# Kernel tuning notes

Measured on AMD Instinct MI355X. Metric: run time of the kernel, lower is better.

Reference implementation:

```python
import jax, jax.numpy as jnp
import numpy as np
import math

B, N, D, L = 2, 256, 128, 4
TD = D // 2  # time embed dim
GROUPS = 32

def _interleave_sincos(v):
    # torch: stack((v[...,0::2].sin(), v[...,1::2].cos()), -1).flatten(last two)
    s = jnp.sin(v[..., 0::2])
    c = jnp.cos(v[..., 1::2])
    return jnp.stack([s, c], axis=-1).reshape(v.shape[:-1] + (-1,))

def _pos_embed(coords):
    # PositionEmbeddingSine(num_pos_feats=D//2, normalize=True, scale=2*pi)
    npf = D // 2
    dim_t = jnp.power(10000.0, 2.0 * jnp.floor(jnp.arange(npf, dtype=jnp.float32) / 2.0) / npf)
    scale = 2.0 * math.pi
    py = _interleave_sincos((coords[:, :, 0] * scale)[:, :, None] / dim_t)
    px = _interleave_sincos((coords[:, :, 1] * scale)[:, :, None] / dim_t)
    return jnp.concatenate([py, px], axis=-1)  # (B,N,D)

def _edge_pos_embed(adj):
    # ScalarEmbeddingSine(num_pos_feats=D, normalize=False)
    dim_t = jnp.power(10000.0, 2.0 * jnp.floor(jnp.arange(D, dtype=jnp.float32) / 2.0) / D)
    return _interleave_sincos(adj[:, :, :, None] / dim_t)  # (B,N,N,D)

def _timestep_embedding(t, dim):
    half = dim // 2
    freqs = jnp.exp(-math.log(10000.0) * jnp.arange(half, dtype=jnp.float32) / half)
    args = t.astype(jnp.float32)[:, None] * freqs
    return jnp.concatenate([jnp.cos(args), jnp.sin(args)], axis=-1)  # (B,D)

def _ln(x, s, b, eps=1e-5):
    mu = jnp.mean(x, -1, keepdims=True)
    var = jnp.var(x, -1, keepdims=True)
    return (x - mu) * jax.lax.rsqrt(var + eps) * s + b

def _gn(x, s, b, groups=GROUPS, eps=1e-5):
    # GroupNorm32 over (B, C, H, W)
    bb, c, h, w = x.shape
    xg = x.reshape(bb, groups, c // groups, h, w)
    mu = jnp.mean(xg, (2, 3, 4), keepdims=True)
    var = jnp.var(xg, (2, 3, 4), keepdims=True)
    xg = (xg - mu) * jax.lax.rsqrt(var + eps)
    return xg.reshape(bb, c, h, w) * s[None, :, None, None] + b[None, :, None, None]

def _forward(coords, adj_t, t, node_W, node_b, edge_W, edge_b, te1_W, te1_b, te2_W, te2_b,
             A_W, A_b, B_W, B_b, C_W, C_b, U_W, U_b, V_W, V_b,
             lnh_s, lnh_b, lne_s, lne_b, tl_W, tl_b,
             plo_ln_s, plo_ln_b, plo_W, plo_b, gn_s, gn_b, conv_W, conv_b):
    x = _pos_embed(coords) @ node_W + node_b            # (B,N,D)
    e = _edge_pos_embed(adj_t) @ edge_W + edge_b        # (B,N,N,D)
    te = _timestep_embedding(t, D) @ te1_W + te1_b
    te = jax.nn.relu(te) @ te2_W + te2_b                # (B,TD)
    for i in range(L):
        x_in, e_in = x, e
        # GatedGCNLayer (mode=direct, no internal residual)
        Uh = x @ U_W[i] + U_b[i]
        Vh = x @ V_W[i] + V_b[i]
        gate_input = ((x @ A_W[i] + A_b[i])[:, :, None, :]
                      + (x @ B_W[i] + B_b[i])[:, None, :, :]
                      + (e @ C_W[i] + C_b[i]))          # (B,N,N,D)
        gates = jax.nn.sigmoid(gate_input)
        agg = jnp.einsum('bijd,bjd->bid', gates, Vh)     # sum over neighbors j
        h_new = jax.nn.relu(_ln(Uh + agg, lnh_s[i], lnh_b[i]))
        e_new = jax.nn.relu(_ln(gate_input, lne_s[i], lne_b[i]))
        # time injection into edges: ReLU -> Linear(TD->D)
        e_new = e_new + (jax.nn.relu(te) @ tl_W[i] + tl_b[i])[:, None, None, :]
        # external residuals + per-layer out (LN -> SiLU -> Linear)
        x = x_in + h_new
        e = e_in + jax.nn.silu(_ln(e_new, plo_ln_s[i], plo_ln_b[i])) @ plo_W[i] + plo_b[i]
    eo = jnp.transpose(e, (0, 3, 1, 2))                  # (B,D,N,N)
    eo = jax.nn.relu(_gn(eo, gn_s, gn_b))
    out = jnp.einsum('bdij,do->boij', eo, conv_W) + conv_b[None, :, None, None]
    return out                                           # (B,1,N,N)

def setup_inputs() -> dict:
    key = jax.random.key(0)
    ks = iter(jax.random.split(key, 64))
    def w(shape, scale=0.02):
        return jax.random.normal(next(ks), shape, dtype=jnp.float32) * scale
    f32 = jnp.float32
    return {
        'coords': jax.random.uniform(next(ks), (B, N, 2), dtype=f32),
        'adj_t': jax.random.normal(next(ks), (B, N, N), dtype=f32),
        't': jax.random.uniform(next(ks), (B,), dtype=f32) * 1000.0,
        'node_W': w((D, D)), 'node_b': jnp.zeros((D,), f32),
        'edge_W': w((D, D)), 'edge_b': jnp.zeros((D,), f32),
        'te1_W': w((D, TD)), 'te1_b': jnp.zeros((TD,), f32),
        'te2_W': w((TD, TD)), 'te2_b': jnp.zeros((TD,), f32),
        'A_W': w((L, D, D)), 'A_b': jnp.zeros((L, D), f32),
        'B_W': w((L, D, D)), 'B_b': jnp.zeros((L, D), f32),
        'C_W': w((L, D, D)), 'C_b': jnp.zeros((L, D), f32),
        'U_W': w((L, D, D)), 'U_b': jnp.zeros((L, D), f32),
        'V_W': w((L, D, D)), 'V_b': jnp.zeros((L, D), f32),
        'lnh_s': jnp.ones((L, D), f32), 'lnh_b': jnp.zeros((L, D), f32),
        'lne_s': jnp.ones((L, D), f32), 'lne_b': jnp.zeros((L, D), f32),
        'tl_W': w((L, TD, D)), 'tl_b': jnp.zeros((L, D), f32),
        'plo_ln_s': jnp.ones((L, D), f32), 'plo_ln_b': jnp.zeros((L, D), f32),
        'plo_W': w((L, D, D)), 'plo_b': jnp.zeros((L, D), f32),
        'gn_s': jnp.ones((D,), f32), 'gn_b': jnp.zeros((D,), f32),
        'conv_W': w((D, 1)), 'conv_b': jnp.zeros((1,), f32),
    }

def reference(coords, adj_t, t, node_W, node_b, edge_W, edge_b, te1_W, te1_b, te2_W, te2_b,
              A_W, A_b, B_W, B_b, C_W, C_b, U_W, U_b, V_W, V_b,
              lnh_s, lnh_b, lne_s, lne_b, tl_W, tl_b,
              plo_ln_s, plo_ln_b, plo_W, plo_b, gn_s, gn_b, conv_W, conv_b):
    return _forward(coords, adj_t, t, node_W, node_b, edge_W, edge_b, te1_W, te1_b, te2_W, te2_b,
                    A_W, A_b, B_W, B_b, C_W, C_b, U_W, U_b, V_W, V_b,
                    lnh_s, lnh_b, lne_s, lne_b, tl_W, tl_b,
                    plo_ln_s, plo_ln_b, plo_W, plo_b, gn_s, gn_b, conv_W, conv_b)
```

## Files before the change

kernel.cpp:

```cpp
#include <hip/hip_runtime.h>
#include <hip/hip_bf16.h>

typedef unsigned short u16;
typedef __attribute__((ext_vector_type(8))) short short8;
typedef __attribute__((ext_vector_type(8))) unsigned short ushort8;
typedef __attribute__((ext_vector_type(4))) float f32x4;

#define BB 2
#define NN 256
#define DD 128
#define TDD 64
#define LL 4
#define NGROUP 32
#define NROWS (BB*NN*NN)
#define LDS_STR 68

#define LOG1E4 9.210340371976184f
#define TWO_PI 6.283185307179586f

#define TILE_GEMM(AT, WPTR, ACC) do {                                          \
  _Pragma("unroll 4")                                                          \
  for (int k = 0; k < 128; ++k) {                                              \
    const float4 w4 = *reinterpret_cast<const float4*>((WPTR) + k*128 + tx*4); \
    const float4 a0 = *reinterpret_cast<const float4*>(&(AT)[k*LDS_STR + ty*8]);     \
    const float4 a1 = *reinterpret_cast<const float4*>(&(AT)[k*LDS_STR + ty*8 + 4]); \
    const float av[8] = {a0.x,a0.y,a0.z,a0.w,a1.x,a1.y,a1.z,a1.w};             \
    const float wv[4] = {w4.x,w4.y,w4.z,w4.w};                                 \
    _Pragma("unroll") for (int r = 0; r < 8; ++r)                              \
      _Pragma("unroll") for (int c = 0; c < 4; ++c)                            \
        ACC[r][c] += av[r]*wv[c];                                              \
  }                                                                            \
} while (0)

__device__ __forceinline__ float sigmoidf_(float x) {
  return 1.f / (1.f + __expf(-x));
}

__device__ __forceinline__ u16 f2bf(float f) {
  union { float f; unsigned int u; } c; c.f = f;
  unsigned int r = (c.u + 0x7FFFu + ((c.u >> 16) & 1u)) >> 16;
  return (u16)r;
}

__global__ __launch_bounds__(512) void k_time(
    const float* __restrict__ t,
    const float* __restrict__ te1_W, const float* __restrict__ te1_b,
    const float* __restrict__ te2_W, const float* __restrict__ te2_b,
    const float* __restrict__ tl_W,  const float* __restrict__ tl_b,
    float* __restrict__ tproj) {
  __shared__ float temb[BB][128], h1[BB][64], rt[BB][64];
  const int tid = threadIdx.x;
  const int b  = tid >> 8;
  const int t2 = tid & 255;
  const float tv = t[b];
  if (t2 < 128) {
    int j = t2 & 63;
    float f = expf(-LOG1E4 * (float)j / 64.f);
    float a = tv * f;
    temb[b][t2] = (t2 < 64) ? cosf(a) : sinf(a);
  }
  __syncthreads();
  if (t2 < 64) {
    float acc = te1_b[t2];
#pragma unroll
    for (int k = 0; k < 128; ++k) acc += temb[b][k] * te1_W[k*64 + t2];
    h1[b][t2] = fmaxf(acc, 0.f);
  }
  __syncthreads();
  if (t2 < 64) {
    float acc = te2_b[t2];
#pragma unroll
    for (int k = 0; k < 64; ++k) acc += h1[b][k] * te2_W[k*64 + t2];
    rt[b][t2] = fmaxf(acc, 0.f);
  }
  __syncthreads();
  if (t2 < 128) {
#pragma unroll
    for (int i = 0; i < LL; ++i) {
      float acc = tl_b[i*128 + t2];
#pragma unroll
      for (int k = 0; k < 64; ++k) acc += rt[b][k] * tl_W[(i*64 + k)*128 + t2];
      tproj[(i*BB + b)*128 + t2] = acc;
    }
  }
}

__global__ __launch_bounds__(256) void k_node_embed(
    const float* __restrict__ coords, const float* __restrict__ W,
    const float* __restrict__ bias, float* __restrict__ x_out) {
  __shared__ float at[128*LDS_STR];
  int tid = threadIdx.x;
  int row = tid >> 2, part = tid & 3;
  int R = blockIdx.x*64 + row;
  float cy = coords[R*2 + 0], cx = coords[R*2 + 1];
#pragma unroll
  for (int q = 0; q < 32; ++q) {
    int c = part*32 + q;
    int k = (c < 64) ? c : c - 64;
    float v = (c < 64) ? cy : cx;
    int m = k >> 1;
    float inv = expf(-LOG1E4 * (float)m / 32.f);
    float a = v * TWO_PI * inv;
    at[c*LDS_STR + row] = (k & 1) ? cosf(a) : sinf(a);
  }
  __syncthreads();
  int tx = tid & 31, ty = tid >> 5;
  float acc[8][4] = {};
  TILE_GEMM(at, W, acc);
  float4 bb4 = *reinterpret_cast<const float4*>(bias + tx*4);
#pragma unroll
  for (int r = 0; r < 8; ++r) {
    int R2 = blockIdx.x*64 + ty*8 + r;
    float4 o = {acc[r][0]+bb4.x, acc[r][1]+bb4.y, acc[r][2]+bb4.z, acc[r][3]+bb4.w};
    *reinterpret_cast<float4*>(x_out + (size_t)R2*128 + tx*4) = o;
  }
}

__global__ __launch_bounds__(256) void k_wprep_e(
    const float* __restrict__ EW, u16* __restrict__ WTE) {
  int idx = blockIdx.x*256 + threadIdx.x;
  int n = idx >> 7, k = idx & 127;
  WTE[n*128 + k] = f2bf(EW[(size_t)k*128 + n]);
}

__global__ __launch_bounds__(256, 3) void k_edge_embed2(
    const float* __restrict__ adj, const u16* __restrict__ WTE,
    const float* __restrict__ bias, float* __restrict__ e_out) {
  __shared__ __align__(16) u16 Abuf[64*128];
  __shared__ __align__(16) u16 Wbuf[128*128];

  const int tid = threadIdx.x;
  const int blk = blockIdx.x;
  const int w  = tid >> 6;
  const int l  = tid & 63;
  const int lg = l >> 4;
  const int ln = l & 15;

  {
    const int r = tid >> 1, h = tid & 1;
    const int r7 = r & 7;
    const u16* src = WTE + r*128;
    u16* dst = Wbuf + r*128;
#pragma unroll
    for (int q = 0; q < 8; ++q) {
      int c = h*8 + q;
      short8 v = *reinterpret_cast<const short8*>(src + c*8);
      *reinterpret_cast<short8*>(dst + ((c ^ r7) << 3)) = v;
    }
  }
  {
    const int r = tid >> 2;
    const int p = tid & 3;
    const float v = adj[(size_t)blk*64 + r];
    const int r7 = r & 7;
    u16* arow = Abuf + r*128;
#pragma unroll
    for (int q = 0; q < 4; ++q) {
      u16 h8[8];
#pragma unroll
      for (int j = 0; j < 8; ++j) {
        int k = (p*4 + q)*8 + j;
        int m = k >> 1;
        float inv = expf(-LOG1E4 * (float)m / 64.f);
        float a = v * inv;
        h8[j] = f2bf((k & 1) ? cosf(a) : sinf(a));
      }
      int pc = (p*4 + q) ^ r7;
      *reinterpret_cast<ushort8*>(arow + pc*8) = *reinterpret_cast<ushort8*>(h8);
    }
  }
  __syncthreads();

  f32x4 acc[8];
#pragma unroll
  for (int nt = 0; nt < 8; ++nt) {
    const float bv = bias[nt*16 + ln];
#pragma unroll
    for (int rg = 0; rg < 4; ++rg) acc[nt][rg] = bv;
  }
  {
    const u16* arow = Abuf + (w*16 + ln)*128;
    const int r7 = ln & 7;
#pragma unroll
    for (int ks = 0; ks < 4; ++ks) {
      short8 a = *reinterpret_cast<const short8*>(arow + (((ks*4 + lg) ^ r7) << 3));
#pragma unroll
      for (int nt = 0; nt < 8; ++nt) {
        short8 bw = *reinterpret_cast<const short8*>(
            Wbuf + (nt*16 + ln)*128 + (((ks*4 + lg) ^ (ln & 7)) << 3));
        acc[nt] = __builtin_amdgcn_mfma_f32_16x16x32_bf16(a, bw, acc[nt], 0, 0, 0);
      }
    }
  }
#pragma unroll
  for (int nt = 0; nt < 8; ++nt)
#pragma unroll
    for (int rg = 0; rg < 4; ++rg)
      e_out[((size_t)blk*64 + w*16 + lg*4 + rg)*128 + nt*16 + ln] = acc[nt][rg];
}

__global__ __launch_bounds__(128) void k_node4(
    const float* __restrict__ x,
    const float* __restrict__ UW, const float* __restrict__ Ub,
    const float* __restrict__ VW, const float* __restrict__ Vb,
    const float* __restrict__ AW, const float* __restrict__ Ab,
    const float* __restrict__ BW, const float* __restrict__ Bb,
    float* __restrict__ Uh, float* __restrict__ Vh,
    float* __restrict__ Axo, float* __restrict__ Bxo) {
  __shared__ float xr[128];
  int R = blockIdx.x, d = threadIdx.x;
  xr[d] = x[(size_t)R*128 + d];
  __syncthreads();
  float au = Ub[d], av = Vb[d], aa = Ab[d], ab = Bb[d];
  for (int k = 0; k < 128; ++k) {
    float xv = xr[k];
    au += xv * UW[k*128 + d];
    av += xv * VW[k*128 + d];
    aa += xv * AW[k*128 + d];
    ab += xv * BW[k*128 + d];
  }
  Uh[(size_t)R*128 + d] = au;
  Vh[(size_t)R*128 + d] = av;
  Axo[(size_t)R*128 + d] = aa;
  Bxo[(size_t)R*128 + d] = ab;
}

__global__ __launch_bounds__(256) void k_wprep(
    const float* __restrict__ CW, const float* __restrict__ PW,
    u16* __restrict__ WTC, u16* __restrict__ WTP) {
  int idx = blockIdx.x*256 + threadIdx.x;
  int m = idx >> 14;
  int r = idx & 16383;
  int layer = m >> 1;
  int n = r >> 7, k = r & 127;
  if ((m & 1) == 0)
    WTC[layer*16384 + n*128 + k] = f2bf(CW[(size_t)layer*16384 + k*128 + n]);
  else
    WTP[layer*16384 + n*128 + k] = f2bf(PW[(size_t)layer*16384 + k*128 + n]);
}

__global__ __launch_bounds__(512, 2) void k_layer(
    float* __restrict__ e,
    const u16* __restrict__ WTC, const u16* __restrict__ WTP,
    const float* __restrict__ Cb, const float* __restrict__ Ax,
    const float* __restrict__ Bx, const float* __restrict__ Vh,
    const float* __restrict__ lnes_g, const float* __restrict__ lneb_g,
    const float* __restrict__ tp_g,
    const float* __restrict__ plos_g, const float* __restrict__ plobl_g,
    const float* __restrict__ plob_g,
    float* __restrict__ aggP) {

  __shared__ __align__(16) u16 Abuf[128*128];
  __shared__ __align__(16) u16 Wbuf[128*128];

  const int tid = threadIdx.x;
  const int blk0 = blockIdx.x;
  const int blk = ((blk0 & 7) << 7) | (blk0 >> 3);
  const int bi  = blk >> 1;
  const int b   = bi >> 8;
  const int jh  = blk & 1;
  const size_t rbase = (size_t)bi*256 + jh*128;

  const int w  = tid >> 6;
  const int l  = tid & 63;
  const int lg = l >> 4;
  const int ln = l & 15;

  {
    const int r = tid >> 2;
    const int p = tid & 3;
    const float* src = e + (rbase + r)*128 + p*32;
    const int r7 = r & 7;
    u16* arow = Abuf + r*128;
#pragma unroll
    for (int q = 0; q < 4; ++q) {
      float4 f0 = *reinterpret_cast<const float4*>(src + q*8);
      float4 f1 = *reinterpret_cast<const float4*>(src + q*8 + 4);
      int pc = (p*4 + q) ^ r7;
      ushort8 h = {f2bf(f0.x),f2bf(f0.y),f2bf(f0.z),f2bf(f0.w),
                   f2bf(f1.x),f2bf(f1.y),f2bf(f1.z),f2bf(f1.w)};
      *reinterpret_cast<ushort8*>(arow + pc*8) = h;
    }
  }
  {
    const int r = tid >> 2;
    const int h = tid & 3;
    const int r7 = r & 7;
    const u16* src = WTC + r*128;
    u16* dst = Wbuf + r*128;
#pragma unroll
    for (int q = 0; q < 4; ++q) {
      int c = h*4 + q;
      short8 v = *reinterpret_cast<const short8*>(src + c*8);
      *reinterpret_cast<short8*>(dst + ((c ^ r7) << 3)) = v;
    }
  }
  __syncthreads();

  const int lrow0 = w*16 + lg*4;
  const int jrow0 = jh*128 + lrow0;

  f32x4 acc[8];
#pragma unroll
  for (int nt = 0; nt < 8; ++nt) {
    const int c = nt*16 + ln;
    const float cbax = Cb[c] + Ax[(size_t)bi*128 + c];
#pragma unroll
    for (int rg = 0; rg < 4; ++rg)
      acc[nt][rg] = cbax + Bx[((size_t)b*256 + jrow0 + rg)*128 + c];
  }

  {
    const u16* arow = Abuf + (w*16 + ln)*128;
    const int r7 = ln & 7;
#pragma unroll
    for (int ks = 0; ks < 4; ++ks) {
      short8 a = *reinterpret_cast<const short8*>(arow + (((ks*4 + lg) ^ r7) << 3));
#pragma unroll
      for (int nt = 0; nt < 8; ++nt) {
        short8 bw = *reinterpret_cast<const short8*>(
            Wbuf + (nt*16 + ln)*128 + (((ks*4 + lg) ^ (ln & 7)) << 3));
        acc[nt] = __builtin_amdgcn_mfma_f32_16x16x32_bf16(a, bw, acc[nt], 0, 0, 0);
      }
    }
  }

  float av[8] = {0.f,0.f,0.f,0.f,0.f,0.f,0.f,0.f};
  float tp_[8], ls_[8], lb_[8], ps_[8], pl_[8];
#pragma unroll
  for (int nt = 0; nt < 8; ++nt) {
    const int c = nt*16 + ln;
    tp_[nt] = tp_g[b*128 + c];
    ls_[nt] = lnes_g[c];  lb_[nt] = lneb_g[c];
    ps_[nt] = plos_g[c];  pl_[nt] = plobl_g[c];
  }

#pragma unroll
  for (int rg = 0; rg < 4; ++rg) {
    float ss = 0.f, s2 = 0.f;
#pragma unroll
    for (int nt = 0; nt < 8; ++nt) { float g = acc[nt][rg]; ss += g; s2 += g*g; }
    ss += __shfl_xor(ss, 1);  s2 += __shfl_xor(s2, 1);
    ss += __shfl_xor(ss, 2);  s2 += __shfl_xor(s2, 2);
    ss += __shfl_xor(ss, 4);  s2 += __shfl_xor(s2, 4);
    ss += __shfl_xor(ss, 8);  s2 += __shfl_xor(s2, 8);
    const float mean = ss * (1.f/128.f);
    const float rs = rsqrtf(s2 * (1.f/128.f) - mean*mean + 1e-5f);
    const size_t vrow = ((size_t)b*256 + jrow0 + rg)*128;
    float s3 = 0.f, s4 = 0.f;
#pragma unroll
    for (int nt = 0; nt < 8; ++nt) {
      const float g = acc[nt][rg];
      av[nt] += Vh[vrow + nt*16 + ln] * sigmoidf_(g);
      float tv = fmaxf((g - mean)*rs*ls_[nt] + lb_[nt], 0.f) + tp_[nt];
      acc[nt][rg] = tv;
      s3 += tv;  s4 += tv*tv;
    }
    s3 += __shfl_xor(s3, 1);  s4 += __shfl_xor(s4, 1);
    s3 += __shfl_xor(s3, 2);  s4 += __shfl_xor(s4, 2);
    s3 += __shfl_xor(s3, 4);  s4 += __shfl_xor(s4, 4);
    s3 += __shfl_xor(s3, 8);  s4 += __shfl_xor(s4, 8);
    const float mean2 = s3 * (1.f/128.f);
    const float rs2 = rsqrtf(s4 * (1.f/128.f) - mean2*mean2 + 1e-5f);
    const int rr = lrow0 + rg;
    const int rr7 = rr & 7;
#pragma unroll
    for (int nt = 0; nt < 8; ++nt) {
      float vv = (acc[nt][rg] - mean2)*rs2*ps_[nt] + pl_[nt];
      vv = vv * sigmoidf_(vv);
      const int cc = nt*16 + ln;
      const int pc = (cc >> 3) ^ rr7;
      Abuf[rr*128 + pc*8 + (cc & 7)] = f2bf(vv);
    }
  }

  __syncthreads();
  {
    const int r = tid >> 2;
    const int h = tid & 3;
    const int r7 = r & 7;
    const u16* src = WTP + r*128;
    u16* dst = Wbuf + r*128;
#pragma unroll
    for (int q = 0; q < 4; ++q) {
      int c = h*4 + q;
      short8 v = *reinterpret_cast<const short8*>(src + c*8);
      *reinterpret_cast<short8*>(dst + ((c ^ r7) << 3)) = v;
    }
  }
  __syncthreads();

  f32x4 acc2[8];
#pragma unroll
  for (int nt = 0; nt < 8; ++nt) acc2[nt] = (f32x4)(0.f);
  {
    const u16* arow = Abuf + (w*16 + ln)*128;
    const int r7 = ln & 7;
#pragma unroll
    for (int ks = 0; ks < 4; ++ks) {
      short8 a = *reinterpret_cast<const short8*>(arow + (((ks*4 + lg) ^ r7) << 3));
#pragma unroll
      for (int nt = 0; nt < 8; ++nt) {
        short8 bw = *reinterpret_cast<const short8*>(
            Wbuf + (nt*16 + ln)*128 + (((ks*4 + lg) ^ (ln & 7)) << 3));
        acc2[nt] = __builtin_amdgcn_mfma_f32_16x16x32_bf16(a, bw, acc2[nt], 0, 0, 0);
      }
    }
  }

#pragma unroll
  for (int nt = 0; nt < 8; ++nt) {
    const float pbv = plob_g[nt*16 + ln];
#pragma unroll
    for (int rg = 0; rg < 4; ++rg) {
      float* ep = e + (rbase + lrow0 + rg)*128 + nt*16 + ln;
      *ep = *ep + acc2[nt][rg] + pbv;
    }
  }

#pragma unroll
  for (int nt = 0; nt < 8; ++nt) {
    float v = av[nt];
    v += __shfl_xor(v, 16);
    v += __shfl_xor(v, 32);
    av[nt] = v;
  }
  if (lg == 0) {
#pragma unroll
    for (int nt = 0; nt < 8; ++nt)
      aggP[((size_t)blk*8 + w)*128 + nt*16 + ln] = av[nt];
  }
}

__global__ __launch_bounds__(128) void k_xupd(
    const float* __restrict__ aggP, const float* __restrict__ Uh,
    const float* __restrict__ lnh_s, const float* __restrict__ lnh_b,
    float* __restrict__ x) {
  int bi = blockIdx.x, d = threadIdx.x;
  float u = Uh[(size_t)bi*128 + d];
#pragma unroll
  for (int st = 0; st < 16; ++st) u += aggP[((size_t)bi*16 + st)*128 + d];
  float s = u, s2 = u*u;
#pragma unroll
  for (int m = 1; m <= 32; m <<= 1) { s += __shfl_xor(s, m); s2 += __shfl_xor(s2, m); }
  __shared__ float red[4];
  int wid = d >> 6;
  if ((d & 63) == 0) { red[wid] = s; red[2 + wid] = s2; }
  __syncthreads();
  s = red[0] + red[1];  s2 = red[2] + red[3];
  float mean = s * (1.f/128.f);
  float rs = rsqrtf(s2 * (1.f/128.f) - mean*mean + 1e-5f);
  x[(size_t)bi*128 + d] += fmaxf((u - mean)*rs*lnh_s[d] + lnh_b[d], 0.f);
}

__global__ __launch_bounds__(128) void k_zero(float* __restrict__ p) {
  p[threadIdx.x] = 0.f;
}

__global__ __launch_bounds__(256) void k_gnstats2(
    const float* __restrict__ e, float* __restrict__ sraw) {
  const int blk = blockIdx.x;
  const int b = blk >> 8;
  const int c = threadIdx.x & 31;
  const int r0 = threadIdx.x >> 5;
  float s = 0.f, s2 = 0.f;
  for (int it = 0; it < 32; ++it) {
    size_t row = (size_t)blk*256 + it*8 + r0;
    float4 f = *reinterpret_cast<const float4*>(e + row*128 + c*4);
    s  += f.x + f.y + f.z + f.w;
    s2 += f.x*f.x + f.y*f.y + f.z*f.z + f.w*f.w;
  }
  __shared__ float red[256], red2[256];
  red[threadIdx.x] = s;  red2[threadIdx.x] = s2;
  __syncthreads();
  if (threadIdx.x < 32) {
    float S = 0.f, S2 = 0.f;
#pragma unroll
    for (int k = 0; k < 8; ++k) { S += red[k*32 + threadIdx.x]; S2 += red2[k*32 + threadIdx.x]; }
    atomicAdd(&sraw[((size_t)b*32 + threadIdx.x)*2],     S);
    atomicAdd(&sraw[((size_t)b*32 + threadIdx.x)*2 + 1], S2);
  }
}

__global__ __launch_bounds__(64) void k_gnfin(
    const float* __restrict__ raw, float* __restrict__ stats) {
  int i = threadIdx.x;
  const float cnt = (float)(NN*NN*4);
  float S  = raw[i*2];
  float S2 = raw[i*2 + 1];
  float mean = S / cnt;
  float var = S2 / cnt - mean*mean;
  stats[i*2]     = mean;
  stats[i*2 + 1] = rsqrtf(var + 1e-5f);
}

__global__ __launch_bounds__(256) void k_out(
    const float* __restrict__ e, const float* __restrict__ stats,
    const float* __restrict__ gn_s, const float* __restrict__ gn_b,
    const float* __restrict__ convW, const float* __restrict__ convb,
    float* __restrict__ out) {
  int tid = threadIdx.x;
  int row = tid >> 2, part = tid & 3;
  size_t R = (size_t)blockIdx.x*64 + row;
  size_t b = R >> 16;
  float acc = 0.f;
  const float4* er = reinterpret_cast<const float4*>(e + R*128 + part*32);
#pragma unroll
  for (int q = 0; q < 8; ++q) {
    float4 f = er[q];
    float fv[4] = {f.x, f.y, f.z, f.w};
#pragma unroll
    for (int lidx = 0; lidx < 4; ++lidx) {
      int c = part*32 + q*4 + lidx;
      int g = c >> 2;
      float mean = stats[(b*NGROUP + g)*2 + 0];
      float rs   = stats[(b*NGROUP + g)*2 + 1];
      float t = (fv[lidx] - mean)*rs*gn_s[c] + gn_b[c];
      acc += fmaxf(t, 0.f) * convW[c];
    }
  }
  acc += __shfl_xor(acc, 1);
  acc += __shfl_xor(acc, 2);
  if (part == 0) out[R] = acc + convb[0];
}

extern "C" void kernel_launch(void* const* d_in, const int* in_sizes, int n_in,
                              void* d_out, int out_size, void* d_ws, size_t ws_size,
                              hipStream_t stream) {
  const float* coords  = (const float*)d_in[0];
  const float* adj_t   = (const float*)d_in[1];
  const float* t       = (const float*)d_in[2];
  const float* node_W  = (const float*)d_in[3];
  const float* node_b  = (const float*)d_in[4];
  const float* edge_W  = (const float*)d_in[5];
  const float* edge_b  = (const float*)d_in[6];
  const float* te1_W   = (const float*)d_in[7];
  const float* te1_b   = (const float*)d_in[8];
  const float* te2_W   = (const float*)d_in[9];
  const float* te2_b   = (const float*)d_in[10];
  const float* A_W     = (const float*)d_in[11];
  const float* A_b     = (const float*)d_in[12];
  const float* B_W     = (const float*)d_in[13];
  const float* B_b     = (const float*)d_in[14];
  const float* C_W     = (const float*)d_in[15];
  const float* C_b     = (const float*)d_in[16];
  const float* U_W     = (const float*)d_in[17];
  const float* U_b     = (const float*)d_in[18];
  const float* V_W     = (const float*)d_in[19];
  const float* V_b     = (const float*)d_in[20];
  const float* lnh_s   = (const float*)d_in[21];
  const float* lnh_b   = (const float*)d_in[22];
  const float* lne_s   = (const float*)d_in[23];
  const float* lne_b   = (const float*)d_in[24];
  const float* tl_W    = (const float*)d_in[25];
  const float* tl_b    = (const float*)d_in[26];
  const float* plo_ln_s= (const float*)d_in[27];
  const float* plo_ln_b= (const float*)d_in[28];
  const float* plo_W   = (const float*)d_in[29];
  const float* plo_b   = (const float*)d_in[30];
  const float* gn_s    = (const float*)d_in[31];
  const float* gn_b    = (const float*)d_in[32];
  const float* conv_W  = (const float*)d_in[33];
  const float* conv_b  = (const float*)d_in[34];

  float* ws    = (float*)d_ws;
  float* e     = ws;
  float* x     = e + (size_t)NROWS*128;
  float* Uh    = x + 65536;
  float* Vh    = Uh + 65536;
  float* Ax    = Vh + 65536;
  float* Bx    = Ax + 65536;
  float* tproj = Bx + 65536;
  float* sraw  = tproj + 1024;
  float* stats = sraw + 128;
  float* aggP  = stats + 128;
  u16*   WTC   = (u16*)(aggP + 1048576);
  u16*   WTP   = WTC + (size_t)LL*16384;
  u16*   WTE   = WTP + (size_t)LL*16384;

  k_zero<<<1, 128, 0, stream>>>(sraw);
  k_wprep<<<512, 256, 0, stream>>>(C_W, plo_W, WTC, WTP);
  k_wprep_e<<<64, 256, 0, stream>>>(edge_W, WTE);
  k_time<<<1, 512, 0, stream>>>(t, te1_W, te1_b, te2_W, te2_b, tl_W, tl_b, tproj);
  k_node_embed<<<8, 256, 0, stream>>>(coords, node_W, node_b, x);
  k_edge_embed2<<<NROWS/64, 256, 0, stream>>>(adj_t, WTE, edge_b, e);

  for (int i = 0; i < LL; ++i) {
    k_node4<<<BB*NN, 128, 0, stream>>>(x,
        U_W + (size_t)i*16384, U_b + i*128,
        V_W + (size_t)i*16384, V_b + i*128,
        A_W + (size_t)i*16384, A_b + i*128,
        B_W + (size_t)i*16384, B_b + i*128,
        Uh, Vh, Ax, Bx);
    k_layer<<<NROWS/128, 512, 0, stream>>>(e,
        WTC + (size_t)i*16384, WTP + (size_t)i*16384,
        C_b + i*128, Ax, Bx, Vh,
        lne_s + i*128, lne_b + i*128,
        tproj + i*BB*128,
        plo_ln_s + i*128, plo_ln_b + i*128, plo_b + i*128,
        aggP);
    k_xupd<<<BB*NN, 128, 0, stream>>>(aggP, Uh, lnh_s + i*128, lnh_b + i*128, x);
  }

  k_gnstats2<<<512, 256, 0, stream>>>(e, sraw);
  k_gnfin<<<1, 64, 0, stream>>>(sraw, stats);
  k_out<<<NROWS/64, 256, 0, stream>>>(e, stats, gn_s, gn_b, conv_W, conv_b,
                                      (float*)d_out);
}
```

Before: 436.0 us.

## Fuse GroupNorm statistics into final layer kernel and prefetch second weight tile

The last k_layer launch now builds the per-group sum and sum-of-squares of the updated edge tensor from registers. It reduces them with shuffles and shared-memory atomics, then adds them to global sraw with atomics, so the separate k_gnstats2 pass over the full edge tensor is removed. The second GEMM's weight tile is also loaded into registers early, which hides global load latency before the LDS write. The cost is extra register pressure, which could hurt occupancy at 512 threads with 2 blocks per SM, plus more atomics on the stats buffers.

```diff
diff --git a/kernel.cpp b/kernel.cpp
--- a/kernel.cpp
+++ b/kernel.cpp
@@ -248,10 +248,11 @@
     const float* __restrict__ tp_g,
     const float* __restrict__ plos_g, const float* __restrict__ plobl_g,
     const float* __restrict__ plob_g,
-    float* __restrict__ aggP) {
+    float* __restrict__ aggP, float* __restrict__ sraw, int do_stats) {
 
   __shared__ __align__(16) u16 Abuf[128*128];
   __shared__ __align__(16) u16 Wbuf[128*128];
+  __shared__ float sgrp[64];
 
   const int tid = threadIdx.x;
   const int blk0 = blockIdx.x;
@@ -294,6 +295,15 @@
       short8 v = *reinterpret_cast<const short8*>(src + c*8);
       *reinterpret_cast<short8*>(dst + ((c ^ r7) << 3)) = v;
     }
+  }
+  short8 wtp[4];
+  {
+    const int r = tid >> 2;
+    const int h = tid & 3;
+    const u16* src = WTP + r*128;
+#pragma unroll
+    for (int q = 0; q < 4; ++q)
+      wtp[q] = *reinterpret_cast<const short8*>(src + (h*4 + q)*8);
   }
   __syncthreads();
 
@@ -379,15 +389,12 @@
     const int r = tid >> 2;
     const int h = tid & 3;
     const int r7 = r & 7;
-    const u16* src = WTP + r*128;
     u16* dst = Wbuf + r*128;
 #pragma unroll
-    for (int q = 0; q < 4; ++q) {
-      int c = h*4 + q;
-      short8 v = *reinterpret_cast<const short8*>(src + c*8);
-      *reinterpret_cast<short8*>(dst + ((c ^ r7) << 3)) = v;
-    }
-  }
+    for (int q = 0; q < 4; ++q)
+      *reinterpret_cast<short8*>(dst + (((h*4 + q) ^ r7) << 3)) = wtp[q];
+  }
+  if (do_stats && tid < 64) sgrp[tid] = 0.f;
   __syncthreads();
 
   f32x4 acc2[8];
@@ -414,8 +421,31 @@
 #pragma unroll
     for (int rg = 0; rg < 4; ++rg) {
       float* ep = e + (rbase + lrow0 + rg)*128 + nt*16 + ln;
-      *ep = *ep + acc2[nt][rg] + pbv;
-    }
+      float v = *ep + acc2[nt][rg] + pbv;
+      *ep = v;
+      acc2[nt][rg] = v;
+    }
+  }
+
+  if (do_stats) {
+#pragma unroll
+    for (int nt = 0; nt < 8; ++nt) {
+      float gs = acc2[nt][0] + acc2[nt][1] + acc2[nt][2] + acc2[nt][3];
+      float gq = acc2[nt][0]*acc2[nt][0] + acc2[nt][1]*acc2[nt][1]
+               + acc2[nt][2]*acc2[nt][2] + acc2[nt][3]*acc2[nt][3];
+      gs += __shfl_xor(gs, 1);  gq += __shfl_xor(gq, 1);
+      gs += __shfl_xor(gs, 2);  gq += __shfl_xor(gq, 2);
+      gs += __shfl_xor(gs, 16); gq += __shfl_xor(gq, 16);
+      gs += __shfl_xor(gs, 32); gq += __shfl_xor(gq, 32);
+      if ((l & 51) == 0) {
+        int g = nt*4 + (ln >> 2);
+        atomicAdd(&sgrp[g*2],     gs);
+        atomicAdd(&sgrp[g*2 + 1], gq);
+      }
+    }
+    __syncthreads();
+    if (tid < 64)
+      atomicAdd(&sraw[(size_t)b*64 + tid], sgrp[tid]);
   }
 
 #pragma unroll
@@ -457,37 +487,13 @@
   p[threadIdx.x] = 0.f;
 }
 
-__global__ __launch_bounds__(256) void k_gnstats2(
-    const float* __restrict__ e, float* __restrict__ sraw) {
-  const int blk = blockIdx.x;
-  const int b = blk >> 8;
-  const int c = threadIdx.x & 31;
-  const int r0 = threadIdx.x >> 5;
-  float s = 0.f, s2 = 0.f;
-  for (int it = 0; it < 32; ++it) {
-    size_t row = (size_t)blk*256 + it*8 + r0;
-    float4 f = *reinterpret_cast<const float4*>(e + row*128 + c*4);
-    s  += f.x + f.y + f.z + f.w;
-    s2 += f.x*f.x + f.y*f.y + f.z*f.z + f.w*f.w;
-  }
-  __shared__ float red[256], red2[256];
-  red[threadIdx.x] = s;  red2[threadIdx.x] = s2;
-  __syncthreads();
-  if (threadIdx.x < 32) {
-    float S = 0.f, S2 = 0.f;
-#pragma unroll
-    for (int k = 0; k < 8; ++k) { S += red[k*32 + threadIdx.x]; S2 += red2[k*32 + threadIdx.x]; }
-    atomicAdd(&sraw[((size_t)b*32 + threadIdx.x)*2],     S);
-    atomicAdd(&sraw[((size_t)b*32 + threadIdx.x)*2 + 1], S2);
-  }
-}
-
 __global__ __launch_bounds__(64) void k_gnfin(
     const float* __restrict__ raw, float* __restrict__ stats) {
   int i = threadIdx.x;
+  int b = i >> 5, g = i & 31;
   const float cnt = (float)(NN*NN*4);
-  float S  = raw[i*2];
-  float S2 = raw[i*2 + 1];
+  float S  = raw[(size_t)b*64 + g*2];
+  float S2 = raw[(size_t)b*64 + g*2 + 1];
   float mean = S / cnt;
   float var = S2 / cnt - mean*mean;
   stats[i*2]     = mean;
@@ -598,11 +604,10 @@
         lne_s + i*128, lne_b + i*128,
         tproj + i*BB*128,
         plo_ln_s + i*128, plo_ln_b + i*128, plo_b + i*128,
-        aggP);
+        aggP, sraw, (i == LL-1) ? 1 : 0);
     k_xupd<<<BB*NN, 128, 0, stream>>>(aggP, Uh, lnh_s + i*128, lnh_b + i*128, x);
   }
 
-  k_gnstats2<<<512, 256, 0, stream>>>(e, sraw);
   k_gnfin<<<1, 64, 0, stream>>>(sraw, stats);
   k_out<<<NROWS/64, 256, 0, stream>>>(e, stats, gn_s, gn_b, conv_W, conv_b,
                                       (float*)d_out);
```

Measured after the change: 456.6 us. 1.05x slower.
